# Performance work log

Hardware: AMD Instinct MI355X
Metric: run time of the kernel (lower is better)

Reference implementation:

```python
import jax, jax.numpy as jnp
import numpy as np

N = 50000      # num nodes
E = 800000     # num edges (no self loops; added in reference like add_remaining_self_loops)
D = 64         # input_dim
H = 128        # hidden_dim
O = 32         # output_dim
EPS = 1.0      # epsilon (privacy)
ALPHA = 0.5
DELTA = 1.0


def setup_inputs() -> dict:
    key = jax.random.key(0)
    ks = jax.random.split(key, 8)
    x = jax.random.normal(ks[0], (N, D), dtype=jnp.float32)
    row = jax.random.randint(ks[1], (E,), 0, N, dtype=jnp.int32)
    off = jax.random.randint(ks[2], (E,), 1, N, dtype=jnp.int32)
    col = (row + off) % N  # guarantees row != col (no pre-existing self loops)
    edge_index = jnp.stack([row, col], axis=0)
    priv_mask = jax.random.bernoulli(ks[3], 0.5, (N,))
    W1 = jax.random.normal(ks[4], (D, H), dtype=jnp.float32) * (1.0 / np.sqrt(D))
    b1 = jnp.zeros((H,), dtype=jnp.float32)
    W2 = jax.random.normal(ks[5], (H, O), dtype=jnp.float32) * (1.0 / np.sqrt(H))
    b2 = jnp.zeros((O,), dtype=jnp.float32)
    return {"x": x, "edge_index": edge_index, "priv_mask": priv_mask,
            "W1": W1, "b1": b1, "W2": W2, "b2": b2}


def _gcn_norm(edge_index, num_nodes, dtype):
    # add_remaining_self_loops + symmetric normalization deg^-1/2[row]*deg^-1/2[col]
    loops = jnp.arange(num_nodes, dtype=edge_index.dtype)
    row = jnp.concatenate([edge_index[0], loops])
    col = jnp.concatenate([edge_index[1], loops])
    deg = jax.ops.segment_sum(jnp.ones(row.shape[0], dtype=dtype), row,
                              num_segments=num_nodes)
    dis = deg ** -0.5  # deg >= 1 thanks to self loops
    norm = dis[row] * dis[col]  # [E+N]
    return row, col, norm


def reference(x, edge_index, priv_mask, W1, b1, W2, b2):
    row, col, norm = _gcn_norm(edge_index, N, x.dtype)
    exp_eps = float(np.exp(EPS))

    # ---- conv1 (GConvDP with per-node bool priv_mask) ----
    x_j = x[row]                                   # [E+N, D] gather
    p = priv_mask[row].astype(x.dtype)[:, None]    # [E+N, 1]
    transformed = ((exp_eps + 1.0) * x_j - 1.0) * (DELTA / (exp_eps - 1.0)) + ALPHA
    msg = norm[:, None] * (p * transformed + (1.0 - p) * x_j)
    h = jax.ops.segment_sum(msg, col, num_segments=N)  # scatter-add aggregate

    h = jax.nn.relu(h @ W1 + b1)
    # F.dropout skipped: reference is deterministic (eval mode)

    # ---- conv2 (called with priv_mask=False, a Python scalar) ----
    # Literal torch semantics: p_j = False -> False*(...) = 0, ~False = -1,
    # so msg = norm * (-x_j).
    msg2 = -norm[:, None] * h[row]                 # [E+N, H]
    h2 = jax.ops.segment_sum(msg2, col, num_segments=N)

    return h2 @ W2 + b2
```

## Files before the change

kernel.cpp:

```cpp
#include <hip/hip_runtime.h>
#include <math.h>

#define C1 2.163953413738653f
#define C0 -0.081976706869326f


typedef __attribute__((ext_vector_type(8))) short bf16x8;
typedef __attribute__((ext_vector_type(4))) float f32x4;

static __device__ __forceinline__ unsigned short f2bf(float f) {
    unsigned b = __float_as_uint(f);
    return (unsigned short)((b + 0x7FFFu + ((b >> 16) & 1u)) >> 16);
}
static __device__ __forceinline__ float bf2f(unsigned short u) {
    return __uint_as_float((unsigned)u << 16);
}
static __device__ __forceinline__ float bfl(unsigned u) { return __uint_as_float(u << 16); }
static __device__ __forceinline__ float bfh(unsigned u) { return __uint_as_float(u & 0xFFFF0000u); }

__global__ __launch_bounds__(1024) void k_hist2(const int* __restrict__ row,
                                                const int* __restrict__ col, int E, int chunk,
                                                int* __restrict__ hist, int* __restrict__ deg,
                                                const float* __restrict__ W1,
                                                const float* __restrict__ W2,
                                                unsigned short* __restrict__ W1b,
                                                unsigned short* __restrict__ W2b) {
    __shared__ int hc[256];
    int t = threadIdx.x, b = blockIdx.x;
    if (t < 256) hc[t] = 0;
    __syncthreads();
    int lo = b * chunk, hi = min(E, lo + chunk);
    int base = lo + t * 4;
    for (; base + 3 < hi; base += 4096) {
        int4 r4 = *(const int4*)&row[base];
        int4 c4 = *(const int4*)&col[base];
        atomicAdd(&hc[c4.x >> 8], 1); atomicAdd(&hc[c4.y >> 8], 1);
        atomicAdd(&hc[c4.z >> 8], 1); atomicAdd(&hc[c4.w >> 8], 1);
        atomicAdd(&deg[r4.x], 1); atomicAdd(&deg[r4.y], 1);
        atomicAdd(&deg[r4.z], 1); atomicAdd(&deg[r4.w], 1);
    }
    for (; base < hi; ++base) {
        atomicAdd(&hc[col[base] >> 8], 1);
        atomicAdd(&deg[row[base]], 1);
    }
    __syncthreads();
    if (t < 256) hist[t * 256 + b] = hc[t];
    if (b == 0) {
        for (int i = t; i < 8192; i += 1024) {
            int j = i & 7, l2 = (i >> 3) & 63, kt = (i >> 9) & 1, nt = i >> 10;
            int k = kt * 32 + (l2 >> 4) * 8 + j, n = nt * 16 + (l2 & 15);
            W1b[i] = f2bf(W1[k * 128 + n]);
        }
    } else if (b == 1) {
        for (int i = t; i < 4096; i += 1024) {
            int j = i & 7, l2 = (i >> 3) & 63, kt = (i >> 9) & 3, nt = i >> 11;
            int k = kt * 32 + (l2 >> 4) * 8 + j, n = nt * 16 + (l2 & 15);
            W2b[i] = f2bf(W2[k * 32 + n]);
        }
    }
}

__global__ __launch_bounds__(256) void k_scan2(const int* __restrict__ cnt,
                                               int* __restrict__ excl,
                                               int* __restrict__ bsum, int n,
                                               const int* __restrict__ deg,
                                               const int* __restrict__ priv,
                                               const float* __restrict__ x, int N,
                                               float* __restrict__ dis,
                                               unsigned short* __restrict__ xt) {
    __shared__ int s[256];
    __shared__ float sdv[256];
    __shared__ int sp[256];
    int t = threadIdx.x;
    if ((int)blockIdx.x < 256) {
        int idx = blockIdx.x * 256 + t;
        int v = (idx < n) ? cnt[idx] : 0;
        s[t] = v;
        __syncthreads();
        for (int off = 1; off < 256; off <<= 1) {
            int u = (t >= off) ? s[t - off] : 0;
            __syncthreads();
            s[t] += u;
            __syncthreads();
        }
        if (idx < n) excl[idx] = s[t] - v;
        if (t == 255) bsum[blockIdx.x] = s[255];
    } else {
        int b2 = blockIdx.x - 256;
        int node = b2 * 256 + t;
        float dv = 0.f;
        int p = 0;
        if (node < N) {
            dv = rsqrtf((float)(deg[node] + 1));
            dis[node] = dv;
            p = priv[node];
        }
        sdv[t] = dv;
        sp[t] = p;
        __syncthreads();
        int basen = b2 * 256;
        for (int i = t; i < 256 * 16; i += 256) {
            int ln = i >> 4;
            int n2 = basen + ln;
            if (n2 >= N) continue;
            float d2 = sdv[ln];
            int pp = sp[ln];
            float4 v = ((const float4*)x)[(size_t)n2 * 16 + (i & 15)];
            float4 tr;
            tr.x = pp ? fmaf(C1, v.x, C0) : v.x;
            tr.y = pp ? fmaf(C1, v.y, C0) : v.y;
            tr.z = pp ? fmaf(C1, v.z, C0) : v.z;
            tr.w = pp ? fmaf(C1, v.w, C0) : v.w;
            ushort4 o;
            o.x = f2bf(d2 * tr.x); o.y = f2bf(d2 * tr.y);
            o.z = f2bf(d2 * tr.z); o.w = f2bf(d2 * tr.w);
            ((ushort4*)xt)[(size_t)n2 * 16 + (i & 15)] = o;
        }
    }
}

__global__ __launch_bounds__(1024) void k_part(const int* __restrict__ row,
                                               const int* __restrict__ col, int E, int chunk,
                                               const int* __restrict__ excl,
                                               const int* __restrict__ bsum,
                                               unsigned* __restrict__ cbuf) {
    __shared__ int sc[256];
    __shared__ int offc[256];
    int t = threadIdx.x, b = blockIdx.x;
    if (t < 256) sc[t] = bsum[t];
    __syncthreads();
    for (int off = 1; off < 256; off <<= 1) {
        int u = (t < 256 && t >= off) ? sc[t - off] : 0;
        __syncthreads();
        if (t < 256) sc[t] += u;
        __syncthreads();
    }
    if (t < 256) offc[t] = sc[t] - bsum[t] + excl[t * 256 + b];
    __syncthreads();
    int lo = b * chunk, hi = min(E, lo + chunk);
    int base = lo + t * 4;
    for (; base + 3 < hi; base += 4096) {
        int4 r4 = *(const int4*)&row[base];
        int4 c4 = *(const int4*)&col[base];
        int p0 = atomicAdd(&offc[c4.x >> 8], 1);
        cbuf[p0] = ((unsigned)c4.x << 16) | (unsigned)r4.x;
        int p1 = atomicAdd(&offc[c4.y >> 8], 1);
        cbuf[p1] = ((unsigned)c4.y << 16) | (unsigned)r4.y;
        int p2 = atomicAdd(&offc[c4.z >> 8], 1);
        cbuf[p2] = ((unsigned)c4.z << 16) | (unsigned)r4.z;
        int p3 = atomicAdd(&offc[c4.w >> 8], 1);
        cbuf[p3] = ((unsigned)c4.w << 16) | (unsigned)r4.w;
    }
    for (; base < hi; ++base) {
        int r = row[base], c = col[base];
        int pc = atomicAdd(&offc[c >> 8], 1);
        cbuf[pc] = ((unsigned)c << 16) | (unsigned)r;
    }
}

__global__ __launch_bounds__(256) void k_csr(const unsigned* __restrict__ cbuf,
                                             const int* __restrict__ bsum, int N,
                                             int* __restrict__ cntC, int* __restrict__ colStart,
                                             unsigned short* __restrict__ eSrc) {
    __shared__ int s1[256], s2[256], s3[256];
    int t = threadIdx.x, b = blockIdx.x;
    s1[t] = (t < b) ? bsum[t] : 0;
    __syncthreads();
    for (int off = 128; off > 0; off >>= 1) {
        if (t < off) s1[t] += s1[t + off];
        __syncthreads();
    }
    int cs = s1[0];
    int ce = cs + bsum[b];
    __syncthreads();
    s1[t] = 0; s3[t] = 0;
    __syncthreads();
    for (int i = cs + t; i < ce; i += 256) atomicAdd(&s1[(cbuf[i] >> 16) & 255], 1);
    __syncthreads();
    int v = s1[t];
    s2[t] = v;
    __syncthreads();
    for (int off = 1; off < 256; off <<= 1) {
        int u = (t >= off) ? s2[t - off] : 0;
        __syncthreads();
        s2[t] += u;
        __syncthreads();
    }
    int excl = s2[t] - v;
    int c = b * 256 + t;
    if (c < N) { cntC[c] = v; colStart[c] = cs + excl; }
    __syncthreads();
    s2[t] = excl;
    __syncthreads();
    for (int i = cs + t; i < ce; i += 256) {
        unsigned e = cbuf[i];
        int d = (e >> 16) & 255;
        int pos = cs + s2[d] + atomicAdd(&s3[d], 1);
        eSrc[pos] = (unsigned short)(e & 0xFFFFu);
    }
}

__global__ __launch_bounds__(256) void k_gather1(const unsigned short* __restrict__ xt,
                                                 const unsigned short* __restrict__ eSrc,
                                                 const int* __restrict__ colStart,
                                                 const int* __restrict__ cntC,
                                                 const float* __restrict__ dis,
                                                 unsigned short* __restrict__ agg1b, int N) {
    int t = blockIdx.x * blockDim.x + threadIdx.x;
    int c = t >> 5, j = t & 31;
    if (c >= N) return;
    const unsigned* x32 = (const unsigned*)xt;
    unsigned u = x32[(size_t)c * 32 + j];
    float s0 = bfl(u), s1 = bfh(u);
    int start = colStart[c], cnt = cntC[c];
    for (int base = 0; base < cnt; base += 32) {
        int m = min(cnt - base, 32);
        int ids = (j < m) ? (int)eSrc[start + base + j] : 0;
        int k = 0;
        for (; k + 8 <= m; k += 8) {
            int r0 = __shfl(ids, k, 32),     r1 = __shfl(ids, k + 1, 32);
            int r2 = __shfl(ids, k + 2, 32), r3 = __shfl(ids, k + 3, 32);
            int r4 = __shfl(ids, k + 4, 32), r5 = __shfl(ids, k + 5, 32);
            int r6 = __shfl(ids, k + 6, 32), r7 = __shfl(ids, k + 7, 32);
            unsigned u0 = x32[(size_t)r0 * 32 + j];
            unsigned u1 = x32[(size_t)r1 * 32 + j];
            unsigned u2 = x32[(size_t)r2 * 32 + j];
            unsigned u3 = x32[(size_t)r3 * 32 + j];
            unsigned u4 = x32[(size_t)r4 * 32 + j];
            unsigned u5 = x32[(size_t)r5 * 32 + j];
            unsigned u6 = x32[(size_t)r6 * 32 + j];
            unsigned u7 = x32[(size_t)r7 * 32 + j];
            s0 += bfl(u0); s1 += bfh(u0);
            s0 += bfl(u1); s1 += bfh(u1);
            s0 += bfl(u2); s1 += bfh(u2);
            s0 += bfl(u3); s1 += bfh(u3);
            s0 += bfl(u4); s1 += bfh(u4);
            s0 += bfl(u5); s1 += bfh(u5);
            s0 += bfl(u6); s1 += bfh(u6);
            s0 += bfl(u7); s1 += bfh(u7);
        }
        for (; k + 4 <= m; k += 4) {
            int r0 = __shfl(ids, k, 32),     r1 = __shfl(ids, k + 1, 32);
            int r2 = __shfl(ids, k + 2, 32), r3 = __shfl(ids, k + 3, 32);
            unsigned u0 = x32[(size_t)r0 * 32 + j];
            unsigned u1 = x32[(size_t)r1 * 32 + j];
            unsigned u2 = x32[(size_t)r2 * 32 + j];
            unsigned u3 = x32[(size_t)r3 * 32 + j];
            s0 += bfl(u0); s1 += bfh(u0);
            s0 += bfl(u1); s1 += bfh(u1);
            s0 += bfl(u2); s1 += bfh(u2);
            s0 += bfl(u3); s1 += bfh(u3);
        }
        for (; k < m; ++k) {
            int r = __shfl(ids, k, 32);
            unsigned uu = x32[(size_t)r * 32 + j];
            s0 += bfl(uu); s1 += bfh(uu);
        }
    }
    float dv = dis[c];
    unsigned o = ((unsigned)f2bf(dv * s1) << 16) | (unsigned)f2bf(dv * s0);
    ((unsigned*)agg1b)[(size_t)c * 32 + j] = o;
}

__global__ __launch_bounds__(256) void k_mlp_mfma(const unsigned short* __restrict__ agg1b,
                                                  const unsigned short* __restrict__ W1b,
                                                  const float* __restrict__ b1,
                                                  const unsigned short* __restrict__ W2b,
                                                  const float* __restrict__ dis,
                                                  unsigned short* __restrict__ hps, int N) {
    __shared__ unsigned short hidA[4][16 * 136];
    const int t = threadIdx.x;
    const int w = t >> 6, l = t & 63;
    const int q = l >> 4, lm = l & 15;
    const int rowbase = blockIdx.x * 64 + w * 16;

    bf16x8 a0, a1;
    {
        int node = rowbase + lm;
        if (node >= N) node = N - 1;
        const bf16x8* pa = (const bf16x8*)(agg1b + (size_t)node * 64);
        a0 = pa[q];
        a1 = pa[4 + q];
    }
    float dvals[4];
    #pragma unroll
    for (int r = 0; r < 4; ++r) {
        int node = rowbase + q * 4 + r;
        dvals[r] = (node < N) ? dis[node] : 0.f;
    }

    const bf16x8* w1f = (const bf16x8*)W1b;
    #pragma unroll
    for (int nt = 0; nt < 8; ++nt) {
        float bv = b1[nt * 16 + lm];
        f32x4 acc = {bv, bv, bv, bv};
        acc = __builtin_amdgcn_mfma_f32_16x16x32_bf16(a0, w1f[(nt * 2 + 0) * 64 + l], acc, 0, 0, 0);
        acc = __builtin_amdgcn_mfma_f32_16x16x32_bf16(a1, w1f[(nt * 2 + 1) * 64 + l], acc, 0, 0, 0);
        #pragma unroll
        for (int r = 0; r < 4; ++r)
            hidA[w][(q * 4 + r) * 136 + nt * 16 + lm] = f2bf(fmaxf(acc[r], 0.f));
    }
    __syncthreads();

    bf16x8 ha[4];
    #pragma unroll
    for (int kt = 0; kt < 4; ++kt)
        ha[kt] = *(const bf16x8*)&hidA[w][lm * 136 + kt * 32 + q * 8];

    const bf16x8* w2f = (const bf16x8*)W2b;
    #pragma unroll
    for (int nt = 0; nt < 2; ++nt) {
        f32x4 acc = {0.f, 0.f, 0.f, 0.f};
        #pragma unroll
        for (int kt = 0; kt < 4; ++kt)
            acc = __builtin_amdgcn_mfma_f32_16x16x32_bf16(ha[kt], w2f[(nt * 4 + kt) * 64 + l], acc, 0, 0, 0);
        #pragma unroll
        for (int r = 0; r < 4; ++r) {
            int node = rowbase + q * 4 + r;
            if (node < N)
                hps[(size_t)node * 32 + nt * 16 + lm] = f2bf(acc[r] * dvals[r]);
        }
    }
}

__global__ __launch_bounds__(256) void k_gather2(const unsigned short* __restrict__ hps,
                                                 const unsigned short* __restrict__ eSrc,
                                                 const int* __restrict__ colStart,
                                                 const int* __restrict__ cntC,
                                                 const float* __restrict__ dis,
                                                 const float* __restrict__ b2,
                                                 float* __restrict__ out, int N) {
    int t = blockIdx.x * blockDim.x + threadIdx.x;
    int c = t >> 4, j = t & 15;
    if (c >= N) return;
    const unsigned* h32 = (const unsigned*)hps;
    unsigned u = h32[(size_t)c * 16 + j];
    float s0 = bfl(u), s1 = bfh(u);
    int start = colStart[c], cnt = cntC[c];
    for (int base = 0; base < cnt; base += 16) {
        int m = min(cnt - base, 16);
        int ids = (j < m) ? (int)eSrc[start + base + j] : 0;
        int k = 0;
        for (; k + 8 <= m; k += 8) {
            int r0 = __shfl(ids, k, 16),     r1 = __shfl(ids, k + 1, 16);
            int r2 = __shfl(ids, k + 2, 16), r3 = __shfl(ids, k + 3, 16);
            int r4 = __shfl(ids, k + 4, 16), r5 = __shfl(ids, k + 5, 16);
            int r6 = __shfl(ids, k + 6, 16), r7 = __shfl(ids, k + 7, 16);
            unsigned u0 = h32[(size_t)r0 * 16 + j];
            unsigned u1 = h32[(size_t)r1 * 16 + j];
            unsigned u2 = h32[(size_t)r2 * 16 + j];
            unsigned u3 = h32[(size_t)r3 * 16 + j];
            unsigned u4 = h32[(size_t)r4 * 16 + j];
            unsigned u5 = h32[(size_t)r5 * 16 + j];
            unsigned u6 = h32[(size_t)r6 * 16 + j];
            unsigned u7 = h32[(size_t)r7 * 16 + j];
            s0 += bfl(u0); s1 += bfh(u0);
            s0 += bfl(u1); s1 += bfh(u1);
            s0 += bfl(u2); s1 += bfh(u2);
            s0 += bfl(u3); s1 += bfh(u3);
            s0 += bfl(u4); s1 += bfh(u4);
            s0 += bfl(u5); s1 += bfh(u5);
            s0 += bfl(u6); s1 += bfh(u6);
            s0 += bfl(u7); s1 += bfh(u7);
        }
        for (; k + 4 <= m; k += 4) {
            int r0 = __shfl(ids, k, 16),     r1 = __shfl(ids, k + 1, 16);
            int r2 = __shfl(ids, k + 2, 16), r3 = __shfl(ids, k + 3, 16);
            unsigned u0 = h32[(size_t)r0 * 16 + j];
            unsigned u1 = h32[(size_t)r1 * 16 + j];
            unsigned u2 = h32[(size_t)r2 * 16 + j];
            unsigned u3 = h32[(size_t)r3 * 16 + j];
            s0 += bfl(u0); s1 += bfh(u0);
            s0 += bfl(u1); s1 += bfh(u1);
            s0 += bfl(u2); s1 += bfh(u2);
            s0 += bfl(u3); s1 += bfh(u3);
        }
        for (; k < m; ++k) {
            int r = __shfl(ids, k, 16);
            unsigned uu = h32[(size_t)r * 16 + j];
            s0 += bfl(uu); s1 += bfh(uu);
        }
    }
    float dv = dis[c];
    float2 bb = ((const float2*)b2)[j];
    float2 o;
    o.x = bb.x - dv * s0;
    o.y = bb.y - dv * s1;
    ((float2*)out)[(size_t)c * 16 + j] = o;
}

extern "C" void kernel_launch(void* const* d_in, const int* in_sizes, int n_in,
                              void* d_out, int out_size, void* d_ws, size_t ws_size,
                              hipStream_t stream) {
    const float* x    = (const float*)d_in[0];
    const int*   ei   = (const int*)d_in[1];
    const int*   priv = (const int*)d_in[2];
    const float* W1   = (const float*)d_in[3];
    const float* b1   = (const float*)d_in[4];
    const float* W2   = (const float*)d_in[5];
    const float* b2   = (const float*)d_in[6];
    float* out = (float*)d_out;

    const int N = in_sizes[2];
    const int E = in_sizes[1] / 2;
    const int* row = ei;
    const int* col = ei + E;

    char* ws = (char*)d_ws;
    size_t off = 0;
    auto take = [&](size_t bytes) { char* p = ws + off; off = (off + bytes + 255) & ~(size_t)255; return p; };
    int*            hist     = (int*)           take((size_t)65536 * 4);
    int*            excl     = (int*)           take((size_t)65536 * 4);
    int*            bsum     = (int*)           take(256 * 4);
    int*            deg      = (int*)           take((size_t)N * 4);
    unsigned short* W1b      = (unsigned short*)take((size_t)8192 * 2);
    unsigned short* W2b      = (unsigned short*)take((size_t)4096 * 2);
    unsigned*       cbuf     = (unsigned*)      take((size_t)E * 4);
    float*          dis      = (float*)         take((size_t)N * 4);
    int*            cntC     = (int*)           take((size_t)N * 4);
    int*            colStart = (int*)           take((size_t)N * 4);
    unsigned short* eSrc     = (unsigned short*)take((size_t)E * 2);
    unsigned short* xt       = (unsigned short*)take((size_t)N * 64 * 2);
    unsigned short* agg1b    = (unsigned short*)take((size_t)N * 64 * 2);
    unsigned short* hps      = (unsigned short*)take((size_t)N * 32 * 2);
    (void)ws_size;

    const int chunk = (((E + 255) / 256) + 3) & ~3;
    const int nbk = (N + 255) / 256;

    hipMemsetAsync(deg, 0, (size_t)N * 4, stream);
    k_hist2   <<<256, 1024, 0, stream>>>(row, col, E, chunk, hist, deg, W1, W2, W1b, W2b);
    k_scan2   <<<256 + nbk, 256, 0, stream>>>(hist, excl, bsum, 65536, deg, priv, x, N, dis, xt);
    k_part    <<<256, 1024, 0, stream>>>(row, col, E, chunk, excl, bsum, cbuf);
    k_csr     <<<nbk, 256, 0, stream>>>(cbuf, bsum, N, cntC, colStart, eSrc);
    k_gather1 <<<((size_t)N * 32 + 255) / 256, 256, 0, stream>>>(xt, eSrc, colStart, cntC, dis, agg1b, N);
    k_mlp_mfma<<<(N + 63) / 64, 256, 0, stream>>>(agg1b, W1b, b1, W2b, dis, hps, N);
    k_gather2 <<<((size_t)N * 16 + 255) / 256, 256, 0, stream>>>(hps, eSrc, colStart, cntC, dis, b2, out, N);
}
```

Baseline: 178.5 us.

## Compute degrees via row bucket partition instead of global atomics

Replaces the global per-node atomic degree counting (and its memset) with a second 256-bucket histogram over row ids, partitioned into a row buffer alongside the column partition. Per-node degrees are then counted in shared memory inside a combined build kernel, which also does the feature transform and the CSR construction in separate block ranges. This removes the 800K scattered global atomics and one launch. In exchange it adds extra histogram, scan and partition traffic for row ids plus a 2-byte row buffer write and read.

```diff
diff --git a/kernel.cpp b/kernel.cpp
--- a/kernel.cpp
+++ b/kernel.cpp
@@ -20,14 +20,14 @@
 
 __global__ __launch_bounds__(1024) void k_hist2(const int* __restrict__ row,
                                                 const int* __restrict__ col, int E, int chunk,
-                                                int* __restrict__ hist, int* __restrict__ deg,
+                                                int* __restrict__ hist,
                                                 const float* __restrict__ W1,
                                                 const float* __restrict__ W2,
                                                 unsigned short* __restrict__ W1b,
                                                 unsigned short* __restrict__ W2b) {
-    __shared__ int hc[256];
+    __shared__ int hc[256], hr[256];
     int t = threadIdx.x, b = blockIdx.x;
-    if (t < 256) hc[t] = 0;
+    if (t < 256) { hc[t] = 0; hr[t] = 0; }
     __syncthreads();
     int lo = b * chunk, hi = min(E, lo + chunk);
     int base = lo + t * 4;
@@ -36,15 +36,18 @@
         int4 c4 = *(const int4*)&col[base];
         atomicAdd(&hc[c4.x >> 8], 1); atomicAdd(&hc[c4.y >> 8], 1);
         atomicAdd(&hc[c4.z >> 8], 1); atomicAdd(&hc[c4.w >> 8], 1);
-        atomicAdd(&deg[r4.x], 1); atomicAdd(&deg[r4.y], 1);
-        atomicAdd(&deg[r4.z], 1); atomicAdd(&deg[r4.w], 1);
+        atomicAdd(&hr[r4.x >> 8], 1); atomicAdd(&hr[r4.y >> 8], 1);
+        atomicAdd(&hr[r4.z >> 8], 1); atomicAdd(&hr[r4.w >> 8], 1);
     }
     for (; base < hi; ++base) {
         atomicAdd(&hc[col[base] >> 8], 1);
-        atomicAdd(&deg[row[base]], 1);
-    }
-    __syncthreads();
-    if (t < 256) hist[t * 256 + b] = hc[t];
+        atomicAdd(&hr[row[base] >> 8], 1);
+    }
+    __syncthreads();
+    if (t < 256) {
+        hist[t * 256 + b] = hc[t];
+        hist[65536 + t * 256 + b] = hr[t];
+    }
     if (b == 0) {
         for (int i = t; i < 8192; i += 1024) {
             int j = i & 7, l2 = (i >> 3) & 63, kt = (i >> 9) & 1, nt = i >> 10;
@@ -60,82 +63,43 @@
     }
 }
 
-__global__ __launch_bounds__(256) void k_scan2(const int* __restrict__ cnt,
-                                               int* __restrict__ excl,
-                                               int* __restrict__ bsum, int n,
-                                               const int* __restrict__ deg,
-                                               const int* __restrict__ priv,
-                                               const float* __restrict__ x, int N,
-                                               float* __restrict__ dis,
-                                               unsigned short* __restrict__ xt) {
+__global__ void k_scan_a(const int* __restrict__ cnt, int* __restrict__ excl,
+                         int* __restrict__ bsum, int n) {
     __shared__ int s[256];
-    __shared__ float sdv[256];
-    __shared__ int sp[256];
-    int t = threadIdx.x;
-    if ((int)blockIdx.x < 256) {
-        int idx = blockIdx.x * 256 + t;
-        int v = (idx < n) ? cnt[idx] : 0;
-        s[t] = v;
-        __syncthreads();
-        for (int off = 1; off < 256; off <<= 1) {
-            int u = (t >= off) ? s[t - off] : 0;
-            __syncthreads();
-            s[t] += u;
-            __syncthreads();
-        }
-        if (idx < n) excl[idx] = s[t] - v;
-        if (t == 255) bsum[blockIdx.x] = s[255];
-    } else {
-        int b2 = blockIdx.x - 256;
-        int node = b2 * 256 + t;
-        float dv = 0.f;
-        int p = 0;
-        if (node < N) {
-            dv = rsqrtf((float)(deg[node] + 1));
-            dis[node] = dv;
-            p = priv[node];
-        }
-        sdv[t] = dv;
-        sp[t] = p;
-        __syncthreads();
-        int basen = b2 * 256;
-        for (int i = t; i < 256 * 16; i += 256) {
-            int ln = i >> 4;
-            int n2 = basen + ln;
-            if (n2 >= N) continue;
-            float d2 = sdv[ln];
-            int pp = sp[ln];
-            float4 v = ((const float4*)x)[(size_t)n2 * 16 + (i & 15)];
-            float4 tr;
-            tr.x = pp ? fmaf(C1, v.x, C0) : v.x;
-            tr.y = pp ? fmaf(C1, v.y, C0) : v.y;
-            tr.z = pp ? fmaf(C1, v.z, C0) : v.z;
-            tr.w = pp ? fmaf(C1, v.w, C0) : v.w;
-            ushort4 o;
-            o.x = f2bf(d2 * tr.x); o.y = f2bf(d2 * tr.y);
-            o.z = f2bf(d2 * tr.z); o.w = f2bf(d2 * tr.w);
-            ((ushort4*)xt)[(size_t)n2 * 16 + (i & 15)] = o;
-        }
-    }
+    int idx = blockIdx.x * 256 + threadIdx.x;
+    int v = (idx < n) ? cnt[idx] : 0;
+    s[threadIdx.x] = v;
+    __syncthreads();
+    for (int off = 1; off < 256; off <<= 1) {
+        int t = (threadIdx.x >= off) ? s[threadIdx.x - off] : 0;
+        __syncthreads();
+        s[threadIdx.x] += t;
+        __syncthreads();
+    }
+    if (idx < n) excl[idx] = s[threadIdx.x] - v;
+    if (threadIdx.x == 255) bsum[blockIdx.x] = s[255];
 }
 
 __global__ __launch_bounds__(1024) void k_part(const int* __restrict__ row,
                                                const int* __restrict__ col, int E, int chunk,
                                                const int* __restrict__ excl,
                                                const int* __restrict__ bsum,
-                                               unsigned* __restrict__ cbuf) {
-    __shared__ int sc[256];
-    __shared__ int offc[256];
+                                               unsigned* __restrict__ cbuf,
+                                               unsigned short* __restrict__ rbuf) {
+    __shared__ int sc[512];
+    __shared__ int offc[256], offr[256];
     int t = threadIdx.x, b = blockIdx.x;
-    if (t < 256) sc[t] = bsum[t];
-    __syncthreads();
+    if (t < 512) sc[t] = bsum[t];
+    __syncthreads();
+    int half = t >> 8, d = t & 255;
     for (int off = 1; off < 256; off <<= 1) {
-        int u = (t < 256 && t >= off) ? sc[t - off] : 0;
-        __syncthreads();
-        if (t < 256) sc[t] += u;
+        int u = (t < 512 && d >= off) ? sc[half * 256 + d - off] : 0;
+        __syncthreads();
+        if (t < 512) sc[t] += u;
         __syncthreads();
     }
     if (t < 256) offc[t] = sc[t] - bsum[t] + excl[t * 256 + b];
+    else if (t < 512) offr[d] = sc[t] - bsum[t] + excl[65536 + d * 256 + b];
     __syncthreads();
     int lo = b * chunk, hi = min(E, lo + chunk);
     int base = lo + t * 4;
@@ -150,53 +114,108 @@
         cbuf[p2] = ((unsigned)c4.z << 16) | (unsigned)r4.z;
         int p3 = atomicAdd(&offc[c4.w >> 8], 1);
         cbuf[p3] = ((unsigned)c4.w << 16) | (unsigned)r4.w;
+        int q0 = atomicAdd(&offr[r4.x >> 8], 1); rbuf[q0] = (unsigned short)r4.x;
+        int q1 = atomicAdd(&offr[r4.y >> 8], 1); rbuf[q1] = (unsigned short)r4.y;
+        int q2 = atomicAdd(&offr[r4.z >> 8], 1); rbuf[q2] = (unsigned short)r4.z;
+        int q3 = atomicAdd(&offr[r4.w >> 8], 1); rbuf[q3] = (unsigned short)r4.w;
     }
     for (; base < hi; ++base) {
         int r = row[base], c = col[base];
         int pc = atomicAdd(&offc[c >> 8], 1);
         cbuf[pc] = ((unsigned)c << 16) | (unsigned)r;
-    }
-}
-
-__global__ __launch_bounds__(256) void k_csr(const unsigned* __restrict__ cbuf,
-                                             const int* __restrict__ bsum, int N,
-                                             int* __restrict__ cntC, int* __restrict__ colStart,
-                                             unsigned short* __restrict__ eSrc) {
+        int pr = atomicAdd(&offr[r >> 8], 1);
+        rbuf[pr] = (unsigned short)r;
+    }
+}
+
+__global__ __launch_bounds__(256) void k_build(const unsigned short* __restrict__ rbuf,
+                                               const unsigned* __restrict__ cbuf,
+                                               const int* __restrict__ bsum,
+                                               const int* __restrict__ priv,
+                                               const float* __restrict__ x, int N, int E, int nbk,
+                                               float* __restrict__ dis,
+                                               unsigned short* __restrict__ xt,
+                                               int* __restrict__ cntC, int* __restrict__ colStart,
+                                               unsigned short* __restrict__ eSrc) {
     __shared__ int s1[256], s2[256], s3[256];
-    int t = threadIdx.x, b = blockIdx.x;
-    s1[t] = (t < b) ? bsum[t] : 0;
-    __syncthreads();
-    for (int off = 128; off > 0; off >>= 1) {
-        if (t < off) s1[t] += s1[t + off];
-        __syncthreads();
-    }
-    int cs = s1[0];
-    int ce = cs + bsum[b];
-    __syncthreads();
-    s1[t] = 0; s3[t] = 0;
-    __syncthreads();
-    for (int i = cs + t; i < ce; i += 256) atomicAdd(&s1[(cbuf[i] >> 16) & 255], 1);
-    __syncthreads();
-    int v = s1[t];
-    s2[t] = v;
-    __syncthreads();
-    for (int off = 1; off < 256; off <<= 1) {
-        int u = (t >= off) ? s2[t - off] : 0;
-        __syncthreads();
-        s2[t] += u;
-        __syncthreads();
-    }
-    int excl = s2[t] - v;
-    int c = b * 256 + t;
-    if (c < N) { cntC[c] = v; colStart[c] = cs + excl; }
-    __syncthreads();
-    s2[t] = excl;
-    __syncthreads();
-    for (int i = cs + t; i < ce; i += 256) {
-        unsigned e = cbuf[i];
-        int d = (e >> 16) & 255;
-        int pos = cs + s2[d] + atomicAdd(&s3[d], 1);
-        eSrc[pos] = (unsigned short)(e & 0xFFFFu);
+    int t = threadIdx.x;
+    if ((int)blockIdx.x < nbk) {
+        int b = blockIdx.x;
+        s1[t] = (t < b) ? bsum[256 + t] : 0;
+        __syncthreads();
+        for (int off = 128; off > 0; off >>= 1) {
+            if (t < off) s1[t] += s1[t + off];
+            __syncthreads();
+        }
+        int rs = s1[0];
+        int re = rs + bsum[256 + b];
+        __syncthreads();
+        s1[t] = 0;
+        __syncthreads();
+        for (int i = rs + t; i < re; i += 256) atomicAdd(&s1[rbuf[i] & 255], 1);
+        __syncthreads();
+        int node = b * 256 + t;
+        float dv = rsqrtf((float)(s1[t] + 1));
+        if (node < N) {
+            dis[node] = dv;
+            s2[t] = __float_as_int(dv);
+            s3[t] = priv[node];
+        } else { s2[t] = 0; s3[t] = 0; }
+        __syncthreads();
+        int base = b * 256;
+        for (int i = t; i < 256 * 16; i += 256) {
+            int ln = i >> 4;
+            int n2 = base + ln;
+            if (n2 >= N) continue;
+            float d2 = __int_as_float(s2[ln]);
+            int p = s3[ln];
+            float4 v = ((const float4*)x)[(size_t)n2 * 16 + (i & 15)];
+            float4 tr;
+            tr.x = p ? fmaf(C1, v.x, C0) : v.x;
+            tr.y = p ? fmaf(C1, v.y, C0) : v.y;
+            tr.z = p ? fmaf(C1, v.z, C0) : v.z;
+            tr.w = p ? fmaf(C1, v.w, C0) : v.w;
+            ushort4 o;
+            o.x = f2bf(d2 * tr.x); o.y = f2bf(d2 * tr.y);
+            o.z = f2bf(d2 * tr.z); o.w = f2bf(d2 * tr.w);
+            ((ushort4*)xt)[(size_t)n2 * 16 + (i & 15)] = o;
+        }
+    } else {
+        int b = blockIdx.x - nbk;
+        s1[t] = (t < b) ? bsum[t] : 0;
+        __syncthreads();
+        for (int off = 128; off > 0; off >>= 1) {
+            if (t < off) s1[t] += s1[t + off];
+            __syncthreads();
+        }
+        int cs = s1[0];
+        int ce = cs + bsum[b];
+        __syncthreads();
+        s1[t] = 0; s3[t] = 0;
+        __syncthreads();
+        for (int i = cs + t; i < ce; i += 256) atomicAdd(&s1[(cbuf[i] >> 16) & 255], 1);
+        __syncthreads();
+        int v = s1[t];
+        s2[t] = v;
+        __syncthreads();
+        for (int off = 1; off < 256; off <<= 1) {
+            int u = (t >= off) ? s2[t - off] : 0;
+            __syncthreads();
+            s2[t] += u;
+            __syncthreads();
+        }
+        int excl = s2[t] - v;
+        int c = b * 256 + t;
+        if (c < N) { cntC[c] = v; colStart[c] = cs + excl; }
+        __syncthreads();
+        s2[t] = excl;
+        __syncthreads();
+        for (int i = cs + t; i < ce; i += 256) {
+            unsigned e = cbuf[i];
+            int d = (e >> 16) & 255;
+            int pos = cs + s2[d] + atomicAdd(&s3[d], 1);
+            eSrc[pos] = (unsigned short)(e & 0xFFFFu);
+        }
     }
 }
 
@@ -409,13 +428,13 @@
     char* ws = (char*)d_ws;
     size_t off = 0;
     auto take = [&](size_t bytes) { char* p = ws + off; off = (off + bytes + 255) & ~(size_t)255; return p; };
-    int*            hist     = (int*)           take((size_t)65536 * 4);
-    int*            excl     = (int*)           take((size_t)65536 * 4);
-    int*            bsum     = (int*)           take(256 * 4);
-    int*            deg      = (int*)           take((size_t)N * 4);
+    int*            hist     = (int*)           take((size_t)131072 * 4);
+    int*            excl     = (int*)           take((size_t)131072 * 4);
+    int*            bsum     = (int*)           take(512 * 4);
     unsigned short* W1b      = (unsigned short*)take((size_t)8192 * 2);
     unsigned short* W2b      = (unsigned short*)take((size_t)4096 * 2);
     unsigned*       cbuf     = (unsigned*)      take((size_t)E * 4);
+    unsigned short* rbuf     = (unsigned short*)take((size_t)E * 2);
     float*          dis      = (float*)         take((size_t)N * 4);
     int*            cntC     = (int*)           take((size_t)N * 4);
     int*            colStart = (int*)           take((size_t)N * 4);
@@ -428,11 +447,11 @@
     const int chunk = (((E + 255) / 256) + 3) & ~3;
     const int nbk = (N + 255) / 256;
 
-    hipMemsetAsync(deg, 0, (size_t)N * 4, stream);
-    k_hist2   <<<256, 1024, 0, stream>>>(row, col, E, chunk, hist, deg, W1, W2, W1b, W2b);
-    k_scan2   <<<256 + nbk, 256, 0, stream>>>(hist, excl, bsum, 65536, deg, priv, x, N, dis, xt);
-    k_part    <<<256, 1024, 0, stream>>>(row, col, E, chunk, excl, bsum, cbuf);
-    k_csr     <<<nbk, 256, 0, stream>>>(cbuf, bsum, N, cntC, colStart, eSrc);
+    k_hist2   <<<256, 1024, 0, stream>>>(row, col, E, chunk, hist, W1, W2, W1b, W2b);
+    k_scan_a  <<<512, 256, 0, stream>>>(hist, excl, bsum, 131072);
+    k_part    <<<256, 1024, 0, stream>>>(row, col, E, chunk, excl, bsum, cbuf, rbuf);
+    k_build   <<<2 * nbk, 256, 0, stream>>>(rbuf, cbuf, bsum, priv, x, N, E, nbk,
+                                            dis, xt, cntC, colStart, eSrc);
     k_gather1 <<<((size_t)N * 32 + 255) / 256, 256, 0, stream>>>(xt, eSrc, colStart, cntC, dis, agg1b, N);
     k_mlp_mfma<<<(N + 63) / 64, 256, 0, stream>>>(agg1b, W1b, b1, W2b, dis, hps, N);
     k_gather2 <<<((size_t)N * 16 + 255) / 256, 256, 0, stream>>>(hps, eSrc, colStart, cntC, dis, b2, out, N);
```

New measurement: 146.5 us. 1.22x faster.
